# Performance work log

Measured on AMD Instinct MI355X. Metric: run time of the kernel, lower is better.

The kernel has to match this reference:

```python
import jax, jax.numpy as jnp
import numpy as np

N, E, F, EF, H = 10000, 320000, 512, 6, 256


def _lin(k, fan_in, fan_out):
    # torch.nn.Linear default init
    s = 1.0 / np.sqrt(fan_in)
    kw, kb = jax.random.split(k)
    W = jax.random.uniform(kw, (fan_in, fan_out), minval=-s, maxval=s, dtype=jnp.float32)
    b = jax.random.uniform(kb, (fan_out,), minval=-s, maxval=s, dtype=jnp.float32)
    return W, b


def setup_inputs() -> dict:
    key = jax.random.key(0)
    ks = jax.random.split(key, 13)
    inp = {}
    inp["x"] = jax.random.normal(ks[0], (N, F), dtype=jnp.float32)
    inp["edge_index"] = jax.random.randint(ks[1], (2, E), 0, N, dtype=jnp.int32)
    inp["edge_attr"] = jax.random.normal(ks[2], (E, EF), dtype=jnp.float32)
    shapes = {
        "We0a": (2 * F + EF, H), "We0b": (H, H),   # conv_in edge MLP
        "Wn0a": (F + H, H),      "Wn0b": (H, H),   # conv_in node MLP
        "We1a": (3 * H, H),      "We1b": (H, H),   # conv[0] edge MLP
        "Wn1a": (2 * H, H),      "Wn1b": (H, H),   # conv[0] node MLP
        "Wp1":  (H, H),          "Wp2":  (H, 1),   # EdgePredictorFromEdges
    }
    for i, (nm, (fi, fo)) in enumerate(shapes.items()):
        W, b = _lin(ks[3 + i % 10], fi, fo)
        inp[nm] = W
        inp["b" + nm[1:]] = b
    return inp


def _mp(x, src, dst, ea, Wea, bea, Web, beb, Wna, bna, Wnb, bnb, residual, agg_mean):
    # MetaLayer edge model: MLP(concat[x_i, x_j, edge_attr])
    e_in = jnp.concatenate([x[src], x[dst], ea], axis=-1)   # [E, ...]
    new_ea = jax.nn.relu(e_in @ Wea + bea) @ Web + beb
    if residual:
        new_ea = new_ea + ea
    # node model: aggregate incoming edges at dst, MLP(concat[x, agg])
    agg = jax.ops.segment_sum(new_ea, dst, num_segments=N)  # [N, H]
    if agg_mean:
        deg = jax.ops.segment_sum(jnp.ones((src.shape[0],), x.dtype), dst, num_segments=N)
        agg = agg / jnp.maximum(deg, 1.0)[:, None]
    n_in = jnp.concatenate([x, agg], axis=-1)
    new_x = jax.nn.relu(n_in @ Wna + bna) @ Wnb + bnb
    if residual:
        new_x = new_x + x
    return new_x, new_ea


def reference(x, edge_index, edge_attr,
              We0a, be0a, We0b, be0b, Wn0a, bn0a, Wn0b, bn0b,
              We1a, be1a, We1b, be1b, Wn1a, bn1a, Wn1b, bn1b,
              Wp1, bp1, Wp2, bp2):
    src, dst = edge_index[0], edge_index[1]
    # conv_in: dims change (F->H, EF->H) so no residual; base_aggregation='mean'
    x1, ea1 = _mp(x, src, dst, edge_attr, We0a, be0a, We0b, be0b,
                  Wn0a, bn0a, Wn0b, bn0b, residual=False, agg_mean=True)
    # conv[0]: dims match -> residual; default base_aggregation='sum'
    x2, ea2 = _mp(x1, src, dst, ea1, We1a, be1a, We1b, be1b,
                  Wn1a, bn1a, Wn1b, bn1b, residual=True, agg_mean=False)
    # EdgePredictorFromEdges (eval mode -> dropout is identity)
    h = jax.nn.leaky_relu(ea2 @ Wp1 + bp1)
    out = (h @ Wp2 + bp2)[:, 0]  # squeeze -> [E]
    return out
```

## Files before the change

kernel.cpp:

```cpp
#include <hip/hip_runtime.h>

#define N_NODES 10000
#define N_EDGES 320000
#define HD      256

typedef __attribute__((ext_vector_type(8))) short bf16x8;
typedef __attribute__((ext_vector_type(4))) float f32x4;
#define MFMA16 __builtin_amdgcn_mfma_f32_16x16x32_bf16

#define OFF_PD    2560000
#define OFF_BA    5120000
#define OFF_BB    7680000
#define OFF_BC    10240000
#define OFF_DEG   12800000
#define OFF_BCV   12810000
#define OFF_PWE0B 12810256
#define OFF_PWEE  (7680000 + 2097152)
#define OFF_PWP1  (OFF_PWEE + 65536)
#define OFF_PWC   (OFF_PWP1 + 65536)
#define OFF_WCF   (OFF_PWC  + 65536)

__device__ __forceinline__ ushort f2bf(float x) {
  union { float f; unsigned u; } c; c.f = x;
  unsigned r = (c.u + 0x7FFFu + ((c.u >> 16) & 1u)) >> 16;
  return (ushort)r;
}
__device__ __forceinline__ float bf2f(ushort h) {
  union { float f; unsigned u; } c; c.u = ((unsigned)h) << 16; return c.f;
}

__global__ __launch_bounds__(256)
void prep_split(const float* __restrict__ W, ushort* __restrict__ H,
                ushort* __restrict__ L)
{
  int slot = blockIdx.x * 256 + threadIdx.x;
  int s    = slot >> 10;
  int rem  = slot & 1023;
  int cf   = rem >> 6;
  int lane = rem & 63;
  int k0 = s * 32 + ((lane >> 4) << 3);
  int n  = cf * 16 + (lane & 15);
#pragma unroll
  for (int j = 0; j < 8; ++j) {
    float v = W[(k0 + j) * HD + n];
    ushort hi = f2bf(v);
    H[slot * 8 + j] = hi;
    L[slot * 8 + j] = f2bf(v - bf2f(hi));
  }
}

__global__ __launch_bounds__(256)
void node_gemm(const float* __restrict__ A1, int K1,
               const float* __restrict__ A2, int K2,
               const float* __restrict__ scale,
               const float* __restrict__ W,
               const float* __restrict__ bias,
               float* __restrict__ C, int M, int act)
{
  __shared__ float sA[64 * 36];
  __shared__ float sB[32 * 256];
  __shared__ float sBias[256];
  const int tid = threadIdx.x;
  const int r0  = blockIdx.x * 64;
  if (bias) sBias[tid] = bias[tid];
  const int ty = tid >> 4, tx = tid & 15;

  float acc[4][16];
#pragma unroll
  for (int r = 0; r < 4; r++)
#pragma unroll
    for (int c = 0; c < 16; c++) acc[r][c] = 0.f;

  const int K = K1 + K2;
  const int arow = tid >> 2;
  const int aks  = (tid & 3) * 8;
  const int gr_a = r0 + arow;

  for (int kb = 0; kb < K; kb += 32) {
    const float* Ap; int lda, koff; float sc = 1.0f;
    if (kb < K1) { Ap = A1; lda = K1; koff = kb; }
    else { Ap = A2; lda = K2; koff = kb - K1;
           if (scale) sc = scale[gr_a < M ? gr_a : M - 1]; }
#pragma unroll
    for (int j = 0; j < 8; j += 4) {
      float4 v;
      if (gr_a < M) v = *(const float4*)&Ap[(long)gr_a * lda + koff + aks + j];
      else { v.x = v.y = v.z = v.w = 0.f; }
      v.x *= sc; v.y *= sc; v.z *= sc; v.w *= sc;
      *(float4*)&sA[arow * 36 + aks + j] = v;
    }
#pragma unroll
    for (int j = 0; j < 8; j++) {
      int i = tid + 256 * j, row = i >> 6, c4 = i & 63;
      *(float4*)&sB[row * HD + c4 * 4] = *(const float4*)&W[(long)(kb + row) * HD + c4 * 4];
    }
    __syncthreads();
#pragma unroll 4
    for (int kk = 0; kk < 32; kk++) {
      float a0 = sA[(ty * 4 + 0) * 36 + kk];
      float a1 = sA[(ty * 4 + 1) * 36 + kk];
      float a2 = sA[(ty * 4 + 2) * 36 + kk];
      float a3 = sA[(ty * 4 + 3) * 36 + kk];
#pragma unroll
      for (int c = 0; c < 16; c++) {
        float b = sB[kk * HD + tx + 16 * c];
        acc[0][c] += a0 * b; acc[1][c] += a1 * b;
        acc[2][c] += a2 * b; acc[3][c] += a3 * b;
      }
    }
    __syncthreads();
  }

#pragma unroll
  for (int r = 0; r < 4; r++) {
    int gr = r0 + ty * 4 + r;
    if (gr >= M) continue;
#pragma unroll
    for (int c = 0; c < 16; c++) {
      int col = tx + 16 * c;
      float v = acc[r][c];
      if (bias) v += sBias[col];
      if (act)  v = fmaxf(v, 0.f);
      C[(long)gr * HD + col] = v;
    }
  }
}

__global__ __launch_bounds__(256)
void bc_k(const float* __restrict__ be1b, const float* __restrict__ Wp1,
          const float* __restrict__ bp1, float* __restrict__ bc)
{
  const int j = threadIdx.x;
  float s = bp1[j];
  for (int k = 0; k < HD; k++) s += be1b[k] * Wp1[k * HD + j];
  bc[j] = s;
}

__global__ void rdeg_k(float* __restrict__ deg)
{
  int i = blockIdx.x * blockDim.x + threadIdx.x;
  if (i < N_NODES) deg[i] = 1.0f / fmaxf(deg[i], 1.0f);
}

__device__ __forceinline__ void build_h0(
    int tid, const float* __restrict__ Ps, const float* __restrict__ Pd,
    const float* sEA, const float* sW6, const float* sB0,
    const int* sSrc, const int* sDst, ushort* Ah, ushort* Al)
{
  const int el = tid >> 4, q = tid & 15;
  const int sv = sSrc[el], dv = sDst[el];
  float eav[6];
#pragma unroll
  for (int k = 0; k < 6; ++k) eav[k] = sEA[el * 6 + k];
  const float* ps = Ps + (long)sv * HD + q * 16;
  const float* pd = Pd + (long)dv * HD + q * 16;
  const int sw = (el & 7) << 4;
  char* ahB = (char*)Ah + el * 512;
  char* alB = (char*)Al + el * 512;
#pragma unroll
  for (int jj = 0; jj < 4; ++jj) {
    float4 a  = *(const float4*)(ps + jj * 4);
    float4 b  = *(const float4*)(pd + jj * 4);
    float4 bb = *(const float4*)(sB0 + q * 16 + jj * 4);
    float vx = a.x + b.x + bb.x;
    float vy = a.y + b.y + bb.y;
    float vz = a.z + b.z + bb.z;
    float vw = a.w + b.w + bb.w;
#pragma unroll
    for (int k = 0; k < 6; ++k) {
      float4 w = *(const float4*)(sW6 + k * HD + q * 16 + jj * 4);
      vx += eav[k] * w.x; vy += eav[k] * w.y;
      vz += eav[k] * w.z; vw += eav[k] * w.w;
    }
    vx = fmaxf(vx, 0.f); vy = fmaxf(vy, 0.f);
    vz = fmaxf(vz, 0.f); vw = fmaxf(vw, 0.f);
    ushort4 hh, ll;
    hh.x = f2bf(vx); hh.y = f2bf(vy); hh.z = f2bf(vz); hh.w = f2bf(vw);
    ll.x = f2bf(vx - bf2f(hh.x)); ll.y = f2bf(vy - bf2f(hh.y));
    ll.z = f2bf(vz - bf2f(hh.z)); ll.w = f2bf(vw - bf2f(hh.w));
    const int off = (q * 32 + jj * 8) ^ sw;
    *(ushort4*)(ahB + off) = hh;
    *(ushort4*)(alB + off) = ll;
  }
}

__device__ __forceinline__ void write_split(ushort* Ah, ushort* Al,
                                            int row, int col, float v)
{
  const int off = row * 512 + ((col * 2) ^ ((row & 7) << 4));
  ushort hi = f2bf(v);
  *(ushort*)((char*)Ah + off) = hi;
  *(ushort*)((char*)Al + off) = f2bf(v - bf2f(hi));
}

__device__ __forceinline__ void gemm_bf3_1(
    const ushort* __restrict__ pH, const ushort* __restrict__ pL,
    ushort* Bs, const ushort* Ah, const ushort* Al,
    int tid, int lane, int wc, int arow, f32x4 acc[4])
{
  const int asw = (arow & 7) << 4;
  for (int s = 0; s < 8; ++s) {
#pragma unroll
    for (int i = 0; i < 2; ++i) {
      int idx16 = tid + (i << 10);
      int c = idx16 >> 6, w16 = idx16 & 63;
      const ushort* src = (c < 16 ? pH : pL) + s * 8192 + (c & 15) * 512 + w16 * 8;
      *(uint4*)(Bs + idx16 * 8) = *(const uint4*)src;
    }
    __syncthreads();
    const int aoff = arow * 512 + (((s << 6) + ((lane >> 4) << 4)) ^ asw);
    bf16x8 ah = *(const bf16x8*)((const char*)Ah + aoff);
    bf16x8 al = *(const bf16x8*)((const char*)Al + aoff);
#pragma unroll
    for (int cf = 0; cf < 4; ++cf) {
      const int cfg = wc * 4 + cf;
      bf16x8 bh = *(const bf16x8*)((const char*)Bs + cfg * 1024 + lane * 16);
      bf16x8 bl = *(const bf16x8*)((const char*)Bs + 16384 + cfg * 1024 + lane * 16);
      acc[cf] = MFMA16(ah, bh, acc[cf], 0, 0, 0);
      acc[cf] = MFMA16(ah, bl, acc[cf], 0, 0, 0);
      acc[cf] = MFMA16(al, bh, acc[cf], 0, 0, 0);
    }
    __syncthreads();
  }
}

__global__ __launch_bounds__(1024)
void edge_conv_in(const int* __restrict__ ei, const float* __restrict__ eattr,
                  const float* __restrict__ Ps, const float* __restrict__ Pd,
                  const float* __restrict__ W6, const float* __restrict__ b0,
                  const ushort* __restrict__ pW0H, const ushort* __restrict__ pW0L,
                  const float* __restrict__ be0b,
                  float* __restrict__ agg, float* __restrict__ deg)
{
  __shared__ ushort Ah[64 * 256];
  __shared__ ushort Al[64 * 256];
  __shared__ ushort Bs[16384];
  __shared__ float  sW6[6 * 256];
  __shared__ float  sEA[64 * 6];
  __shared__ float  sB0[256];
  __shared__ int    sSrc[64], sDst[64];
  const int tid = threadIdx.x;
  const long e0 = (long)blockIdx.x * 64;

  if (tid < 64) {
    int dv = ei[N_EDGES + e0 + tid];
    sDst[tid] = dv;
    atomicAdd(&deg[dv], 1.0f);
  } else if (tid < 128) {
    sSrc[tid - 64] = ei[e0 + tid - 64];
  }
  if (tid < 96)  *(float4*)&sEA[tid * 4] = *(const float4*)&eattr[e0 * 6 + tid * 4];
  if (tid < 384) *(float4*)&sW6[tid * 4] = *(const float4*)&W6[tid * 4];
  if (tid < 64)  *(float4*)&sB0[tid * 4] = *(const float4*)&b0[tid * 4];
  __syncthreads();

  build_h0(tid, Ps, Pd, sEA, sW6, sB0, sSrc, sDst, Ah, Al);
  __syncthreads();

  const int lane = tid & 63, wid = tid >> 6;
  const int wr = wid & 3, wc = wid >> 2;
  const int arow = wr * 16 + (lane & 15);

  f32x4 acc[4];
#pragma unroll
  for (int cf = 0; cf < 4; ++cf) acc[cf] = (f32x4){0.f, 0.f, 0.f, 0.f};
  gemm_bf3_1(pW0H, pW0L, Bs, Ah, Al, tid, lane, wc, arow, acc);

  const int rbase = wr * 16 + ((lane >> 4) << 2);
#pragma unroll
  for (int cf = 0; cf < 4; ++cf) {
    const int col = wc * 64 + cf * 16 + (lane & 15);
    const float bv = be0b[col];
#pragma unroll
    for (int r = 0; r < 4; ++r) {
      const int row = rbase + r;
      atomicAdd(&agg[(long)sDst[row] * HD + col], acc[cf][r] + bv);
    }
  }
}

__global__ __launch_bounds__(1024)
void edge_pred(const int* __restrict__ ei, const float* __restrict__ eattr,
               const float* __restrict__ Ps, const float* __restrict__ Pd,
               const float* __restrict__ W6, const float* __restrict__ b0,
               const ushort* __restrict__ pW0H, const ushort* __restrict__ pW0L,
               const float* __restrict__ be0b,
               const float* __restrict__ P1s, const float* __restrict__ P1d,
               const ushort* __restrict__ pWeE, const ushort* __restrict__ pWp1,
               const ushort* __restrict__ pWc,
               const float* __restrict__ be1a, const float* __restrict__ bc,
               const float* __restrict__ Wp2, const float* __restrict__ bp2,
               float* __restrict__ out)
{
  __shared__ ushort Ah[64 * 256];
  __shared__ ushort Al[64 * 256];
  __shared__ ushort Bs[32768];
  __shared__ float  sW6[6 * 256];
  __shared__ float  sEA[64 * 6];
  __shared__ float  sB0[256];
  __shared__ float  sOut[64];
  __shared__ int    sSrc[64], sDst[64];
  const int tid = threadIdx.x;
  const long e0 = (long)blockIdx.x * 64;

  if (tid < 64) {
    sDst[tid] = ei[N_EDGES + e0 + tid];
    sOut[tid] = bp2[0];
  } else if (tid < 128) {
    sSrc[tid - 64] = ei[e0 + tid - 64];
  }
  if (tid < 96)  *(float4*)&sEA[tid * 4] = *(const float4*)&eattr[e0 * 6 + tid * 4];
  if (tid < 384) *(float4*)&sW6[tid * 4] = *(const float4*)&W6[tid * 4];
  if (tid < 64)  *(float4*)&sB0[tid * 4] = *(const float4*)&b0[tid * 4];
  __syncthreads();

  build_h0(tid, Ps, Pd, sEA, sW6, sB0, sSrc, sDst, Ah, Al);
  __syncthreads();

  const int lane = tid & 63, wid = tid >> 6;
  const int wr = wid & 3, wc = wid >> 2;
  const int arow = wr * 16 + (lane & 15);
  const int asw  = (arow & 7) << 4;
  const int rbase = wr * 16 + ((lane >> 4) << 2);

  {
    f32x4 acc[4];
#pragma unroll
    for (int cf = 0; cf < 4; ++cf) acc[cf] = (f32x4){0.f, 0.f, 0.f, 0.f};
    gemm_bf3_1(pW0H, pW0L, Bs, Ah, Al, tid, lane, wc, arow, acc);
#pragma unroll
    for (int cf = 0; cf < 4; ++cf) {
      const int col = wc * 64 + cf * 16 + (lane & 15);
      const float bv = be0b[col];
#pragma unroll
      for (int r = 0; r < 4; ++r)
        write_split(Ah, Al, rbase + r, col, acc[cf][r] + bv);
    }
  }

  f32x4 acc1[4], accT[4];
#pragma unroll
  for (int cf = 0; cf < 4; ++cf) {
    acc1[cf] = (f32x4){0.f, 0.f, 0.f, 0.f};
    accT[cf] = (f32x4){0.f, 0.f, 0.f, 0.f};
  }
  for (int s = 0; s < 8; ++s) {
#pragma unroll
    for (int i = 0; i < 4; ++i) {
      int idx16 = tid + (i << 10);
      int c = idx16 >> 6, w16 = idx16 & 63;
      const ushort* base = (c < 32 ? pWeE : pWp1) + ((c >> 4) & 1) * 65536;
      const ushort* src = base + s * 8192 + (c & 15) * 512 + w16 * 8;
      *(uint4*)(Bs + idx16 * 8) = *(const uint4*)src;
    }
    __syncthreads();
    const int aoff = arow * 512 + (((s << 6) + ((lane >> 4) << 4)) ^ asw);
    bf16x8 ah = *(const bf16x8*)((const char*)Ah + aoff);
    bf16x8 al = *(const bf16x8*)((const char*)Al + aoff);
#pragma unroll
    for (int cf = 0; cf < 4; ++cf) {
      const int cfg = wc * 4 + cf;
      bf16x8 b1h = *(const bf16x8*)((const char*)Bs + cfg * 1024 + lane * 16);
      bf16x8 b1l = *(const bf16x8*)((const char*)Bs + 16384 + cfg * 1024 + lane * 16);
      bf16x8 b2h = *(const bf16x8*)((const char*)Bs + 32768 + cfg * 1024 + lane * 16);
      bf16x8 b2l = *(const bf16x8*)((const char*)Bs + 49152 + cfg * 1024 + lane * 16);
      acc1[cf] = MFMA16(ah, b1h, acc1[cf], 0, 0, 0);
      acc1[cf] = MFMA16(ah, b1l, acc1[cf], 0, 0, 0);
      acc1[cf] = MFMA16(al, b1h, acc1[cf], 0, 0, 0);
      accT[cf] = MFMA16(ah, b2h, accT[cf], 0, 0, 0);
      accT[cf] = MFMA16(ah, b2l, accT[cf], 0, 0, 0);
      accT[cf] = MFMA16(al, b2h, accT[cf], 0, 0, 0);
    }
    __syncthreads();
  }

#pragma unroll
  for (int cf = 0; cf < 4; ++cf) {
    const int col = wc * 64 + cf * 16 + (lane & 15);
    const float bv = be1a[col];
#pragma unroll
    for (int r = 0; r < 4; ++r) {
      const int row = rbase + r;
      float v = acc1[cf][r] + P1s[(long)sSrc[row] * HD + col]
                            + P1d[(long)sDst[row] * HD + col] + bv;
      write_split(Ah, Al, row, col, fmaxf(v, 0.f));
    }
  }

  f32x4 accZ[4];
#pragma unroll
  for (int cf = 0; cf < 4; ++cf) accZ[cf] = (f32x4){0.f, 0.f, 0.f, 0.f};
  gemm_bf3_1(pWc, pWc + 65536, Bs, Ah, Al, tid, lane, wc, arow, accZ);

  float p[4] = {0.f, 0.f, 0.f, 0.f};
#pragma unroll
  for (int cf = 0; cf < 4; ++cf) {
    const int col = wc * 64 + cf * 16 + (lane & 15);
    const float w   = Wp2[col];
    const float bcv = bc[col];
#pragma unroll
    for (int r = 0; r < 4; ++r) {
      float z = accZ[cf][r] + accT[cf][r] + bcv;
      z = z > 0.f ? z : 0.01f * z;
      p[r] += z * w;
    }
  }
#pragma unroll
  for (int r = 0; r < 4; ++r) {
    p[r] += __shfl_xor(p[r], 1);
    p[r] += __shfl_xor(p[r], 2);
    p[r] += __shfl_xor(p[r], 4);
    p[r] += __shfl_xor(p[r], 8);
  }
  if ((lane & 15) == 0) {
#pragma unroll
    for (int r = 0; r < 4; ++r) atomicAdd(&sOut[rbase + r], p[r]);
  }
  __syncthreads();
  if (tid < 64) out[e0 + tid] = sOut[tid];
}

extern "C" void kernel_launch(void* const* d_in, const int* in_sizes, int n_in,
                              void* d_out, int out_size, void* d_ws, size_t ws_size,
                              hipStream_t stream)
{
  const float* x     = (const float*)d_in[0];
  const int*   ei    = (const int*)d_in[1];
  const float* eattr = (const float*)d_in[2];
  const float* We0a  = (const float*)d_in[3];
  const float* be0a  = (const float*)d_in[4];
  const float* We0b  = (const float*)d_in[5];
  const float* be0b  = (const float*)d_in[6];
  const float* Wn0a  = (const float*)d_in[7];
  const float* bn0a  = (const float*)d_in[8];
  const float* Wn0b  = (const float*)d_in[9];
  const float* bn0b  = (const float*)d_in[10];
  const float* We1a  = (const float*)d_in[11];
  const float* be1a  = (const float*)d_in[12];
  const float* We1b  = (const float*)d_in[13];
  const float* be1b  = (const float*)d_in[14];
  const float* Wp1   = (const float*)d_in[19];
  const float* bp1   = (const float*)d_in[20];
  const float* Wp2   = (const float*)d_in[21];
  const float* bp2   = (const float*)d_in[22];
  float* out = (float*)d_out;
  float* ws  = (float*)d_ws;

  float* P_s  = ws;
  float* P_d  = ws + OFF_PD;
  float* bufA = ws + OFF_BA;
  float* bufB = ws + OFF_BB;
  float* bufC = ws + OFF_BC;
  float* deg  = ws + OFF_DEG;
  float* bcB  = ws + OFF_BCV;
  ushort* pW0  = (ushort*)(ws + OFF_PWE0B);
  ushort* pWeE = (ushort*)(ws + OFF_PWEE);
  ushort* pWp1 = (ushort*)(ws + OFF_PWP1);
  ushort* pWc  = (ushort*)(ws + OFF_PWC);
  float*  WcF  = ws + OFF_WCF;

  const float* W6  = We0a + 1024 * HD;
  const float* WeE = We1a + 512 * HD;

  hipMemsetAsync(bufC, 0, (2560000 + 10000) * sizeof(float), stream);

  const int ngrid = (N_NODES + 63) / 64;
  const int egrid = N_EDGES / 64;

  node_gemm<<<ngrid, 256, 0, stream>>>(x, 512, nullptr, 0, nullptr, We0a,            nullptr, P_s, N_NODES, 0);
  node_gemm<<<ngrid, 256, 0, stream>>>(x, 512, nullptr, 0, nullptr, We0a + 512 * HD, nullptr, P_d, N_NODES, 0);
  prep_split<<<32, 256, 0, stream>>>(We0b, pW0, pW0 + 65536);
  bc_k<<<1, 256, 0, stream>>>(be1b, Wp1, bp1, bcB);

  edge_conv_in<<<egrid, 1024, 0, stream>>>(ei, eattr, P_s, P_d, W6, be0a,
                                           pW0, pW0 + 65536, be0b, bufC, deg);
  rdeg_k<<<(N_NODES + 255) / 256, 256, 0, stream>>>(deg);

  node_gemm<<<ngrid, 256, 0, stream>>>(x, 512, bufC, 256, deg, Wn0a, bn0a, bufA, N_NODES, 1);
  node_gemm<<<ngrid, 256, 0, stream>>>(bufA, 256, nullptr, 0, nullptr, Wn0b, bn0b, bufB, N_NODES, 0);
  node_gemm<<<ngrid, 256, 0, stream>>>(bufB, 256, nullptr, 0, nullptr, We1a,            nullptr, bufA, N_NODES, 0);
  node_gemm<<<ngrid, 256, 0, stream>>>(bufB, 256, nullptr, 0, nullptr, We1a + 256 * HD, nullptr, bufC, N_NODES, 0);

  node_gemm<<<4, 256, 0, stream>>>(We1b, 256, nullptr, 0, nullptr, Wp1, nullptr, WcF, 256, 0);
  prep_split<<<32, 256, 0, stream>>>(WeE, pWeE, pWeE + 65536);
  prep_split<<<32, 256, 0, stream>>>(Wp1, pWp1, pWp1 + 65536);
  prep_split<<<32, 256, 0, stream>>>(WcF, pWc,  pWc  + 65536);

  edge_pred<<<egrid, 1024, 0, stream>>>(ei, eattr, P_s, P_d, W6, be0a,
      pW0, pW0 + 65536, be0b, bufA, bufC, pWeE, pWp1, pWc,
      be1a, bcB, Wp2, bp2, out);
}
```

Baseline: 2.468 ms.

## Fold We0b into downstream weights and drop LDS B staging in edge kernels

Edge_pred no longer recomputes the conv_in second GEMM. We0b is pre-multiplied into WeE and Wp1 (and be0b folded into biases), which removes one 256x256 split-bf16 GEMM per edge tile. Both edge kernels now read pre-packed B fragments straight from global/L2 instead of staging them through LDS with barriers. They also use 512-thread blocks where each wave handles two row blocks, to reuse B fragments and raise occupancy. Folding the weights changes rounding slightly, since products are computed in fp32 and then split to bf16 pairs.

```diff
diff --git a/kernel.cpp b/kernel.cpp
--- a/kernel.cpp
+++ b/kernel.cpp
@@ -8,17 +8,14 @@
 typedef __attribute__((ext_vector_type(4))) float f32x4;
 #define MFMA16 __builtin_amdgcn_mfma_f32_16x16x32_bf16
 
-#define OFF_PD    2560000
-#define OFF_BA    5120000
-#define OFF_BB    7680000
-#define OFF_BC    10240000
-#define OFF_DEG   12800000
-#define OFF_BCV   12810000
-#define OFF_PWE0B 12810256
-#define OFF_PWEE  (7680000 + 2097152)
-#define OFF_PWP1  (OFF_PWEE + 65536)
-#define OFF_PWC   (OFF_PWP1 + 65536)
-#define OFF_WCF   (OFF_PWC  + 65536)
+#define OFF_PD   2560000
+#define OFF_BA   5120000
+#define OFF_BB   7680000
+#define OFF_BC   10240000
+#define OFF_DEG  12800000
+#define OFF_BCV  12810000
+#define OFF_BAV  12810256
+#define OFF_PW0  12810512
 
 __device__ __forceinline__ ushort f2bf(float x) {
   union { float f; unsigned u; } c; c.f = x;
@@ -127,13 +124,17 @@
 }
 
 __global__ __launch_bounds__(256)
-void bc_k(const float* __restrict__ be1b, const float* __restrict__ Wp1,
-          const float* __restrict__ bp1, float* __restrict__ bc)
+void bias_fold_k(const float* __restrict__ v1, const float* __restrict__ v2,
+                 const float* __restrict__ W, const float* __restrict__ base,
+                 float* __restrict__ out)
 {
   const int j = threadIdx.x;
-  float s = bp1[j];
-  for (int k = 0; k < HD; k++) s += be1b[k] * Wp1[k * HD + j];
-  bc[j] = s;
+  float s = base[j];
+  for (int k = 0; k < HD; k++) {
+    float v = v1[k] + (v2 ? v2[k] : 0.f);
+    s += v * W[k * HD + j];
+  }
+  out[j] = s;
 }
 
 __global__ void rdeg_k(float* __restrict__ deg)
@@ -147,28 +148,28 @@
     const float* sEA, const float* sW6, const float* sB0,
     const int* sSrc, const int* sDst, ushort* Ah, ushort* Al)
 {
-  const int el = tid >> 4, q = tid & 15;
+  const int el = tid >> 3, q = tid & 7;
   const int sv = sSrc[el], dv = sDst[el];
   float eav[6];
 #pragma unroll
   for (int k = 0; k < 6; ++k) eav[k] = sEA[el * 6 + k];
-  const float* ps = Ps + (long)sv * HD + q * 16;
-  const float* pd = Pd + (long)dv * HD + q * 16;
+  const float* ps = Ps + (long)sv * HD + q * 32;
+  const float* pd = Pd + (long)dv * HD + q * 32;
   const int sw = (el & 7) << 4;
   char* ahB = (char*)Ah + el * 512;
   char* alB = (char*)Al + el * 512;
 #pragma unroll
-  for (int jj = 0; jj < 4; ++jj) {
+  for (int jj = 0; jj < 8; ++jj) {
     float4 a  = *(const float4*)(ps + jj * 4);
     float4 b  = *(const float4*)(pd + jj * 4);
-    float4 bb = *(const float4*)(sB0 + q * 16 + jj * 4);
+    float4 bb = *(const float4*)(sB0 + q * 32 + jj * 4);
     float vx = a.x + b.x + bb.x;
     float vy = a.y + b.y + bb.y;
     float vz = a.z + b.z + bb.z;
     float vw = a.w + b.w + bb.w;
 #pragma unroll
     for (int k = 0; k < 6; ++k) {
-      float4 w = *(const float4*)(sW6 + k * HD + q * 16 + jj * 4);
+      float4 w = *(const float4*)(sW6 + k * HD + q * 32 + jj * 4);
       vx += eav[k] * w.x; vy += eav[k] * w.y;
       vz += eav[k] * w.z; vw += eav[k] * w.w;
     }
@@ -178,7 +179,7 @@
     hh.x = f2bf(vx); hh.y = f2bf(vy); hh.z = f2bf(vz); hh.w = f2bf(vw);
     ll.x = f2bf(vx - bf2f(hh.x)); ll.y = f2bf(vy - bf2f(hh.y));
     ll.z = f2bf(vz - bf2f(hh.z)); ll.w = f2bf(vw - bf2f(hh.w));
-    const int off = (q * 32 + jj * 8) ^ sw;
+    const int off = (q * 64 + jj * 8) ^ sw;
     *(ushort4*)(ahB + off) = hh;
     *(ushort4*)(alB + off) = ll;
   }
@@ -193,48 +194,24 @@
   *(ushort*)((char*)Al + off) = f2bf(v - bf2f(hi));
 }
 
-__device__ __forceinline__ void gemm_bf3_1(
-    const ushort* __restrict__ pH, const ushort* __restrict__ pL,
-    ushort* Bs, const ushort* Ah, const ushort* Al,
-    int tid, int lane, int wc, int arow, f32x4 acc[4])
-{
-  const int asw = (arow & 7) << 4;
-  for (int s = 0; s < 8; ++s) {
-#pragma unroll
-    for (int i = 0; i < 2; ++i) {
-      int idx16 = tid + (i << 10);
-      int c = idx16 >> 6, w16 = idx16 & 63;
-      const ushort* src = (c < 16 ? pH : pL) + s * 8192 + (c & 15) * 512 + w16 * 8;
-      *(uint4*)(Bs + idx16 * 8) = *(const uint4*)src;
-    }
-    __syncthreads();
-    const int aoff = arow * 512 + (((s << 6) + ((lane >> 4) << 4)) ^ asw);
-    bf16x8 ah = *(const bf16x8*)((const char*)Ah + aoff);
-    bf16x8 al = *(const bf16x8*)((const char*)Al + aoff);
-#pragma unroll
-    for (int cf = 0; cf < 4; ++cf) {
-      const int cfg = wc * 4 + cf;
-      bf16x8 bh = *(const bf16x8*)((const char*)Bs + cfg * 1024 + lane * 16);
-      bf16x8 bl = *(const bf16x8*)((const char*)Bs + 16384 + cfg * 1024 + lane * 16);
-      acc[cf] = MFMA16(ah, bh, acc[cf], 0, 0, 0);
-      acc[cf] = MFMA16(ah, bl, acc[cf], 0, 0, 0);
-      acc[cf] = MFMA16(al, bh, acc[cf], 0, 0, 0);
-    }
-    __syncthreads();
-  }
-}
-
-__global__ __launch_bounds__(1024)
+__device__ __forceinline__ void load_afrag(const ushort* Ah, const ushort* Al,
+    int row, int s, int lane, bf16x8& ah, bf16x8& al)
+{
+  const int aoff = row * 512 + ((((s << 6) + ((lane >> 4) << 4))) ^ ((row & 7) << 4));
+  ah = *(const bf16x8*)((const char*)Ah + aoff);
+  al = *(const bf16x8*)((const char*)Al + aoff);
+}
+
+__global__ __launch_bounds__(512, 4)
 void edge_conv_in(const int* __restrict__ ei, const float* __restrict__ eattr,
                   const float* __restrict__ Ps, const float* __restrict__ Pd,
                   const float* __restrict__ W6, const float* __restrict__ b0,
-                  const ushort* __restrict__ pW0H, const ushort* __restrict__ pW0L,
+                  const ushort* __restrict__ pW0,
                   const float* __restrict__ be0b,
                   float* __restrict__ agg, float* __restrict__ deg)
 {
   __shared__ ushort Ah[64 * 256];
   __shared__ ushort Al[64 * 256];
-  __shared__ ushort Bs[16384];
   __shared__ float  sW6[6 * 256];
   __shared__ float  sEA[64 * 6];
   __shared__ float  sB0[256];
@@ -258,43 +235,63 @@
   __syncthreads();
 
   const int lane = tid & 63, wid = tid >> 6;
-  const int wr = wid & 3, wc = wid >> 2;
-  const int arow = wr * 16 + (lane & 15);
-
-  f32x4 acc[4];
-#pragma unroll
-  for (int cf = 0; cf < 4; ++cf) acc[cf] = (f32x4){0.f, 0.f, 0.f, 0.f};
-  gemm_bf3_1(pW0H, pW0L, Bs, Ah, Al, tid, lane, wc, arow, acc);
-
-  const int rbase = wr * 16 + ((lane >> 4) << 2);
-#pragma unroll
-  for (int cf = 0; cf < 4; ++cf) {
-    const int col = wc * 64 + cf * 16 + (lane & 15);
-    const float bv = be0b[col];
-#pragma unroll
-    for (int r = 0; r < 4; ++r) {
-      const int row = rbase + r;
-      atomicAdd(&agg[(long)sDst[row] * HD + col], acc[cf][r] + bv);
-    }
-  }
-}
-
-__global__ __launch_bounds__(1024)
+  const int wc = wid & 3, wrg = wid >> 2;
+  const bf16x8* pH = (const bf16x8*)pW0;
+  const bf16x8* pL = (const bf16x8*)(pW0 + 65536);
+
+  f32x4 acc[2][4];
+#pragma unroll
+  for (int rb = 0; rb < 2; ++rb)
+#pragma unroll
+    for (int cf = 0; cf < 4; ++cf) acc[rb][cf] = (f32x4){0.f, 0.f, 0.f, 0.f};
+
+#pragma unroll 2
+  for (int s = 0; s < 8; ++s) {
+    bf16x8 ah[2], al[2];
+#pragma unroll
+    for (int rb = 0; rb < 2; ++rb)
+      load_afrag(Ah, Al, (wrg * 2 + rb) * 16 + (lane & 15), s, lane, ah[rb], al[rb]);
+#pragma unroll
+    for (int cf = 0; cf < 4; ++cf) {
+      const int slot = s * 1024 + (wc * 4 + cf) * 64 + lane;
+      bf16x8 bh = pH[slot];
+      bf16x8 bl = pL[slot];
+#pragma unroll
+      for (int rb = 0; rb < 2; ++rb) {
+        acc[rb][cf] = MFMA16(al[rb], bh, acc[rb][cf], 0, 0, 0);
+        acc[rb][cf] = MFMA16(ah[rb], bl, acc[rb][cf], 0, 0, 0);
+        acc[rb][cf] = MFMA16(ah[rb], bh, acc[rb][cf], 0, 0, 0);
+      }
+    }
+  }
+
+#pragma unroll
+  for (int rb = 0; rb < 2; ++rb) {
+    const int rbase = (wrg * 2 + rb) * 16 + ((lane >> 4) << 2);
+#pragma unroll
+    for (int cf = 0; cf < 4; ++cf) {
+      const int col = wc * 64 + cf * 16 + (lane & 15);
+      const float bv = be0b[col];
+#pragma unroll
+      for (int r = 0; r < 4; ++r)
+        atomicAdd(&agg[(long)sDst[rbase + r] * HD + col], acc[rb][cf][r] + bv);
+    }
+  }
+}
+
+__global__ __launch_bounds__(512, 4)
 void edge_pred(const int* __restrict__ ei, const float* __restrict__ eattr,
                const float* __restrict__ Ps, const float* __restrict__ Pd,
                const float* __restrict__ W6, const float* __restrict__ b0,
-               const ushort* __restrict__ pW0H, const ushort* __restrict__ pW0L,
-               const float* __restrict__ be0b,
                const float* __restrict__ P1s, const float* __restrict__ P1d,
-               const ushort* __restrict__ pWeE, const ushort* __restrict__ pWp1,
+               const ushort* __restrict__ pWA, const ushort* __restrict__ pWB,
                const ushort* __restrict__ pWc,
-               const float* __restrict__ be1a, const float* __restrict__ bc,
+               const float* __restrict__ bA, const float* __restrict__ bc,
                const float* __restrict__ Wp2, const float* __restrict__ bp2,
                float* __restrict__ out)
 {
   __shared__ ushort Ah[64 * 256];
   __shared__ ushort Al[64 * 256];
-  __shared__ ushort Bs[32768];
   __shared__ float  sW6[6 * 256];
   __shared__ float  sEA[64 * 6];
   __shared__ float  sB0[256];
@@ -318,103 +315,124 @@
   __syncthreads();
 
   const int lane = tid & 63, wid = tid >> 6;
-  const int wr = wid & 3, wc = wid >> 2;
-  const int arow = wr * 16 + (lane & 15);
-  const int asw  = (arow & 7) << 4;
-  const int rbase = wr * 16 + ((lane >> 4) << 2);
-
-  {
-    f32x4 acc[4];
-#pragma unroll
-    for (int cf = 0; cf < 4; ++cf) acc[cf] = (f32x4){0.f, 0.f, 0.f, 0.f};
-    gemm_bf3_1(pW0H, pW0L, Bs, Ah, Al, tid, lane, wc, arow, acc);
+  const int wc = wid & 3, wrg = wid >> 2;
+  const bf16x8* pAH = (const bf16x8*)pWA;
+  const bf16x8* pAL = (const bf16x8*)(pWA + 65536);
+  const bf16x8* pBH = (const bf16x8*)pWB;
+  const bf16x8* pBL = (const bf16x8*)(pWB + 65536);
+  const bf16x8* pCH = (const bf16x8*)pWc;
+  const bf16x8* pCL = (const bf16x8*)(pWc + 65536);
+
+  f32x4 acc1[2][4], accT[2][4];
+#pragma unroll
+  for (int rb = 0; rb < 2; ++rb)
+#pragma unroll
+    for (int cf = 0; cf < 4; ++cf) {
+      acc1[rb][cf] = (f32x4){0.f, 0.f, 0.f, 0.f};
+      accT[rb][cf] = (f32x4){0.f, 0.f, 0.f, 0.f};
+    }
+
+#pragma unroll 2
+  for (int s = 0; s < 8; ++s) {
+    bf16x8 ah[2], al[2];
+#pragma unroll
+    for (int rb = 0; rb < 2; ++rb)
+      load_afrag(Ah, Al, (wrg * 2 + rb) * 16 + (lane & 15), s, lane, ah[rb], al[rb]);
+#pragma unroll
+    for (int cf = 0; cf < 4; ++cf) {
+      const int slot = s * 1024 + (wc * 4 + cf) * 64 + lane;
+      bf16x8 b1h = pAH[slot];
+      bf16x8 b1l = pAL[slot];
+      bf16x8 b2h = pBH[slot];
+      bf16x8 b2l = pBL[slot];
+#pragma unroll
+      for (int rb = 0; rb < 2; ++rb) {
+        acc1[rb][cf] = MFMA16(al[rb], b1h, acc1[rb][cf], 0, 0, 0);
+        acc1[rb][cf] = MFMA16(ah[rb], b1l, acc1[rb][cf], 0, 0, 0);
+        acc1[rb][cf] = MFMA16(ah[rb], b1h, acc1[rb][cf], 0, 0, 0);
+        accT[rb][cf] = MFMA16(al[rb], b2h, accT[rb][cf], 0, 0, 0);
+        accT[rb][cf] = MFMA16(ah[rb], b2l, accT[rb][cf], 0, 0, 0);
+        accT[rb][cf] = MFMA16(ah[rb], b2h, accT[rb][cf], 0, 0, 0);
+      }
+    }
+  }
+  __syncthreads();
+
+#pragma unroll
+  for (int rb = 0; rb < 2; ++rb) {
+    const int rbase = (wrg * 2 + rb) * 16 + ((lane >> 4) << 2);
 #pragma unroll
     for (int cf = 0; cf < 4; ++cf) {
       const int col = wc * 64 + cf * 16 + (lane & 15);
-      const float bv = be0b[col];
-#pragma unroll
-      for (int r = 0; r < 4; ++r)
-        write_split(Ah, Al, rbase + r, col, acc[cf][r] + bv);
-    }
-  }
-
-  f32x4 acc1[4], accT[4];
-#pragma unroll
-  for (int cf = 0; cf < 4; ++cf) {
-    acc1[cf] = (f32x4){0.f, 0.f, 0.f, 0.f};
-    accT[cf] = (f32x4){0.f, 0.f, 0.f, 0.f};
-  }
+      const float bv = bA[col];
+#pragma unroll
+      for (int r = 0; r < 4; ++r) {
+        const int row = rbase + r;
+        float v = acc1[rb][cf][r] + P1s[(long)sSrc[row] * HD + col]
+                                  + P1d[(long)sDst[row] * HD + col] + bv;
+        write_split(Ah, Al, row, col, fmaxf(v, 0.f));
+      }
+    }
+  }
+  __syncthreads();
+
+  f32x4 accZ[2][4];
+#pragma unroll
+  for (int rb = 0; rb < 2; ++rb)
+#pragma unroll
+    for (int cf = 0; cf < 4; ++cf) accZ[rb][cf] = (f32x4){0.f, 0.f, 0.f, 0.f};
+
+#pragma unroll 2
   for (int s = 0; s < 8; ++s) {
-#pragma unroll
-    for (int i = 0; i < 4; ++i) {
-      int idx16 = tid + (i << 10);
-      int c = idx16 >> 6, w16 = idx16 & 63;
-      const ushort* base = (c < 32 ? pWeE : pWp1) + ((c >> 4) & 1) * 65536;
-      const ushort* src = base + s * 8192 + (c & 15) * 512 + w16 * 8;
-      *(uint4*)(Bs + idx16 * 8) = *(const uint4*)src;
-    }
-    __syncthreads();
-    const int aoff = arow * 512 + (((s << 6) + ((lane >> 4) << 4)) ^ asw);
-    bf16x8 ah = *(const bf16x8*)((const char*)Ah + aoff);
-    bf16x8 al = *(const bf16x8*)((const char*)Al + aoff);
+    bf16x8 ah[2], al[2];
+#pragma unroll
+    for (int rb = 0; rb < 2; ++rb)
+      load_afrag(Ah, Al, (wrg * 2 + rb) * 16 + (lane & 15), s, lane, ah[rb], al[rb]);
 #pragma unroll
     for (int cf = 0; cf < 4; ++cf) {
-      const int cfg = wc * 4 + cf;
-      bf16x8 b1h = *(const bf16x8*)((const char*)Bs + cfg * 1024 + lane * 16);
-      bf16x8 b1l = *(const bf16x8*)((const char*)Bs + 16384 + cfg * 1024 + lane * 16);
-      bf16x8 b2h = *(const bf16x8*)((const char*)Bs + 32768 + cfg * 1024 + lane * 16);
-      bf16x8 b2l = *(const bf16x8*)((const char*)Bs + 49152 + cfg * 1024 + lane * 16);
-      acc1[cf] = MFMA16(ah, b1h, acc1[cf], 0, 0, 0);
-      acc1[cf] = MFMA16(ah, b1l, acc1[cf], 0, 0, 0);
-      acc1[cf] = MFMA16(al, b1h, acc1[cf], 0, 0, 0);
-      accT[cf] = MFMA16(ah, b2h, accT[cf], 0, 0, 0);
-      accT[cf] = MFMA16(ah, b2l, accT[cf], 0, 0, 0);
-      accT[cf] = MFMA16(al, b2h, accT[cf], 0, 0, 0);
-    }
-    __syncthreads();
-  }
-
-#pragma unroll
-  for (int cf = 0; cf < 4; ++cf) {
-    const int col = wc * 64 + cf * 16 + (lane & 15);
-    const float bv = be1a[col];
-#pragma unroll
-    for (int r = 0; r < 4; ++r) {
-      const int row = rbase + r;
-      float v = acc1[cf][r] + P1s[(long)sSrc[row] * HD + col]
-                            + P1d[(long)sDst[row] * HD + col] + bv;
-      write_split(Ah, Al, row, col, fmaxf(v, 0.f));
-    }
-  }
-
-  f32x4 accZ[4];
-#pragma unroll
-  for (int cf = 0; cf < 4; ++cf) accZ[cf] = (f32x4){0.f, 0.f, 0.f, 0.f};
-  gemm_bf3_1(pWc, pWc + 65536, Bs, Ah, Al, tid, lane, wc, arow, accZ);
-
-  float p[4] = {0.f, 0.f, 0.f, 0.f};
+      const int slot = s * 1024 + (wc * 4 + cf) * 64 + lane;
+      bf16x8 bh = pCH[slot];
+      bf16x8 bl = pCL[slot];
+#pragma unroll
+      for (int rb = 0; rb < 2; ++rb) {
+        accZ[rb][cf] = MFMA16(al[rb], bh, accZ[rb][cf], 0, 0, 0);
+        accZ[rb][cf] = MFMA16(ah[rb], bl, accZ[rb][cf], 0, 0, 0);
+        accZ[rb][cf] = MFMA16(ah[rb], bh, accZ[rb][cf], 0, 0, 0);
+      }
+    }
+  }
+
+  float p[2][4] = {{0.f,0.f,0.f,0.f},{0.f,0.f,0.f,0.f}};
 #pragma unroll
   for (int cf = 0; cf < 4; ++cf) {
     const int col = wc * 64 + cf * 16 + (lane & 15);
     const float w   = Wp2[col];
     const float bcv = bc[col];
 #pragma unroll
+    for (int rb = 0; rb < 2; ++rb)
+#pragma unroll
+      for (int r = 0; r < 4; ++r) {
+        float z = accZ[rb][cf][r] + accT[rb][cf][r] + bcv;
+        z = z > 0.f ? z : 0.01f * z;
+        p[rb][r] += z * w;
+      }
+  }
+#pragma unroll
+  for (int rb = 0; rb < 2; ++rb)
+#pragma unroll
     for (int r = 0; r < 4; ++r) {
-      float z = accZ[cf][r] + accT[cf][r] + bcv;
-      z = z > 0.f ? z : 0.01f * z;
-      p[r] += z * w;
-    }
-  }
-#pragma unroll
-  for (int r = 0; r < 4; ++r) {
-    p[r] += __shfl_xor(p[r], 1);
-    p[r] += __shfl_xor(p[r], 2);
-    p[r] += __shfl_xor(p[r], 4);
-    p[r] += __shfl_xor(p[r], 8);
-  }
+      p[rb][r] += __shfl_xor(p[rb][r], 1);
+      p[rb][r] += __shfl_xor(p[rb][r], 2);
+      p[rb][r] += __shfl_xor(p[rb][r], 4);
+      p[rb][r] += __shfl_xor(p[rb][r], 8);
+    }
   if ((lane & 15) == 0) {
 #pragma unroll
-    for (int r = 0; r < 4; ++r) atomicAdd(&sOut[rbase + r], p[r]);
+    for (int rb = 0; rb < 2; ++rb) {
+      const int rbase = (wrg * 2 + rb) * 16 + ((lane >> 4) << 2);
+#pragma unroll
+      for (int r = 0; r < 4; ++r) atomicAdd(&sOut[rbase + r], p[rb][r]);
+    }
   }
   __syncthreads();
   if (tid < 64) out[e0 + tid] = sOut[tid];
@@ -453,11 +471,15 @@
   float* bufC = ws + OFF_BC;
   float* deg  = ws + OFF_DEG;
   float* bcB  = ws + OFF_BCV;
-  ushort* pW0  = (ushort*)(ws + OFF_PWE0B);
-  ushort* pWeE = (ushort*)(ws + OFF_PWEE);
-  ushort* pWp1 = (ushort*)(ws + OFF_PWP1);
-  ushort* pWc  = (ushort*)(ws + OFF_PWC);
-  float*  WcF  = ws + OFF_WCF;
+  float* bAB  = ws + OFF_BAV;
+  ushort* pW0 = (ushort*)(ws + OFF_PW0);
+
+  float*  WAf = ws + OFF_BB;
+  float*  WBf = ws + OFF_BB + 65536;
+  float*  WcF = ws + OFF_BB + 131072;
+  ushort* pWA = (ushort*)(ws + OFF_BB + 196608);
+  ushort* pWB = (ushort*)(ws + OFF_BB + 262144);
+  ushort* pWc = (ushort*)(ws + OFF_BB + 327680);
 
   const float* W6  = We0a + 1024 * HD;
   const float* WeE = We1a + 512 * HD;
@@ -470,10 +492,11 @@
   node_gemm<<<ngrid, 256, 0, stream>>>(x, 512, nullptr, 0, nullptr, We0a,            nullptr, P_s, N_NODES, 0);
   node_gemm<<<ngrid, 256, 0, stream>>>(x, 512, nullptr, 0, nullptr, We0a + 512 * HD, nullptr, P_d, N_NODES, 0);
   prep_split<<<32, 256, 0, stream>>>(We0b, pW0, pW0 + 65536);
-  bc_k<<<1, 256, 0, stream>>>(be1b, Wp1, bp1, bcB);
-
-  edge_conv_in<<<egrid, 1024, 0, stream>>>(ei, eattr, P_s, P_d, W6, be0a,
-                                           pW0, pW0 + 65536, be0b, bufC, deg);
+  bias_fold_k<<<1, 256, 0, stream>>>(be1b, be0b, Wp1, bp1, bcB);
+  bias_fold_k<<<1, 256, 0, stream>>>(be0b, nullptr, WeE, be1a, bAB);
+
+  edge_conv_in<<<egrid, 512, 0, stream>>>(ei, eattr, P_s, P_d, W6, be0a,
+                                          pW0, be0b, bufC, deg);
   rdeg_k<<<(N_NODES + 255) / 256, 256, 0, stream>>>(deg);
 
   node_gemm<<<ngrid, 256, 0, stream>>>(x, 512, bufC, 256, deg, Wn0a, bn0a, bufA, N_NODES, 1);
@@ -481,12 +504,13 @@
   node_gemm<<<ngrid, 256, 0, stream>>>(bufB, 256, nullptr, 0, nullptr, We1a,            nullptr, bufA, N_NODES, 0);
   node_gemm<<<ngrid, 256, 0, stream>>>(bufB, 256, nullptr, 0, nullptr, We1a + 256 * HD, nullptr, bufC, N_NODES, 0);
 
+  node_gemm<<<4, 256, 0, stream>>>(We0b, 256, nullptr, 0, nullptr, WeE, nullptr, WAf, 256, 0);
+  node_gemm<<<4, 256, 0, stream>>>(We0b, 256, nullptr, 0, nullptr, Wp1, nullptr, WBf, 256, 0);
   node_gemm<<<4, 256, 0, stream>>>(We1b, 256, nullptr, 0, nullptr, Wp1, nullptr, WcF, 256, 0);
-  prep_split<<<32, 256, 0, stream>>>(WeE, pWeE, pWeE + 65536);
-  prep_split<<<32, 256, 0, stream>>>(Wp1, pWp1, pWp1 + 65536);
-  prep_split<<<32, 256, 0, stream>>>(WcF, pWc,  pWc  + 65536);
-
-  edge_pred<<<egrid, 1024, 0, stream>>>(ei, eattr, P_s, P_d, W6, be0a,
-      pW0, pW0 + 65536, be0b, bufA, bufC, pWeE, pWp1, pWc,
-      be1a, bcB, Wp2, bp2, out);
-}
+  prep_split<<<32, 256, 0, stream>>>(WAf, pWA, pWA + 65536);
+  prep_split<<<32, 256, 0, stream>>>(WBf, pWB, pWB + 65536);
+  prep_split<<<32, 256, 0, stream>>>(WcF, pWc, pWc + 65536);
+
+  edge_pred<<<egrid, 512, 0, stream>>>(ei, eattr, P_s, P_d, W6, be0a,
+      bufA, bufC, pWA, pWB, pWc, bAB, bcB, Wp2, bp2, out);
+}
```

After: 2.222 ms. -10.0%, faster.
